# Performance work log

Hardware: AMD Instinct MI355X
Metric: run time of the kernel (lower is better)

Reference implementation:

```python
import jax, jax.numpy as jnp
import numpy as np

NUM_HEADS = 32
NUM_KV_HEADS = 8
HEAD_DIM = 64
D_MODEL = 2048
N_REP = NUM_HEADS // NUM_KV_HEADS


def _rotate_half(t):
    h = t.shape[-1] // 2
    return jnp.concatenate([-t[..., h:], t[..., :h]], axis=-1)


def _apply_rope(t, cos, sin):
    # t: (B, H, L, hd); cos/sin: (L, hd) -> broadcast over B, H
    return t * cos[None, None, :, :] + _rotate_half(t) * sin[None, None, :, :]


def setup_inputs() -> dict:
    key = jax.random.key(0)
    ks = jax.random.split(key, 7)
    B, L = 2, 2048
    x = jax.random.normal(ks[0], (B, L, D_MODEL), dtype=jnp.float32)
    # RoPE tables (build real rotary tables for realism)
    inv_freq = 1.0 / (10000.0 ** (jnp.arange(0, HEAD_DIM, 2, dtype=jnp.float32) / HEAD_DIM))
    t = jnp.arange(L, dtype=jnp.float32)
    freqs = jnp.outer(t, inv_freq)              # (L, hd/2)
    emb = jnp.concatenate([freqs, freqs], -1)   # (L, hd)
    cos = jnp.cos(emb)
    sin = jnp.sin(emb)
    s = 0.02
    Wq = s * jax.random.normal(ks[1], (D_MODEL, D_MODEL), dtype=jnp.float32)
    Wk = s * jax.random.normal(ks[2], (NUM_KV_HEADS * HEAD_DIM, D_MODEL), dtype=jnp.float32)
    Wv = s * jax.random.normal(ks[3], (NUM_KV_HEADS * HEAD_DIM, D_MODEL), dtype=jnp.float32)
    Wo = s * jax.random.normal(ks[4], (D_MODEL, D_MODEL), dtype=jnp.float32)
    return {"x": x, "cos": cos, "sin": sin, "Wq": Wq, "Wk": Wk, "Wv": Wv, "Wo": Wo}


def reference(x, cos, sin, Wq, Wk, Wv, Wo):
    B, L, _ = x.shape
    # Projections (Linear: y = x @ W^T)
    Q = (x @ Wq.T).reshape(B, L, NUM_HEADS, HEAD_DIM).transpose(0, 2, 1, 3)      # (B,H,L,d)
    K = (x @ Wk.T).reshape(B, L, NUM_KV_HEADS, HEAD_DIM).transpose(0, 2, 1, 3)   # (B,Hk,L,d)
    V = (x @ Wv.T).reshape(B, L, NUM_KV_HEADS, HEAD_DIM).transpose(0, 2, 1, 3)
    Q = _apply_rope(Q, cos, sin)
    K = _apply_rope(K, cos, sin)
    # GQA: group Q heads by kv head instead of materializing repeated K/V
    Qg = Q.reshape(B, NUM_KV_HEADS, N_REP, L, HEAD_DIM)
    scale = 1.0 / jnp.sqrt(jnp.array(HEAD_DIM, dtype=x.dtype))
    scores = jnp.einsum('bgrqd,bgkd->bgrqk', Qg, K) * scale                      # (B,Hk,rep,L,L)
    causal = jnp.tril(jnp.ones((L, L), dtype=bool))
    scores = jnp.where(causal[None, None, None], scores, jnp.finfo(scores.dtype).min)
    probs = jax.nn.softmax(scores, axis=-1)
    out = jnp.einsum('bgrqk,bgkd->bgrqd', probs, V)                              # (B,Hk,rep,L,d)
    out = out.reshape(B, NUM_HEADS, L, HEAD_DIM).transpose(0, 2, 1, 3).reshape(B, L, D_MODEL)
    return out @ Wo.T
```

## Files before the change

### kernel.cpp

```cpp
#include <hip/hip_runtime.h>
#include <stdint.h>

#define B_   2
#define L_   2048
#define DM   2048
#define NH   32
#define NKV  8
#define HD   64

typedef __attribute__((ext_vector_type(8))) short short8;
typedef __attribute__((ext_vector_type(4))) float f32x4;
typedef __attribute__((ext_vector_type(16))) float f32x16;

__device__ __forceinline__ unsigned short f2b(float f) {
  union { float f; unsigned int u; } x; x.f = f;
  unsigned int u = x.u + 0x7fffu + ((x.u >> 16) & 1u);
  return (unsigned short)(u >> 16);
}

__device__ __forceinline__ void gload16(const void* g, void* l) {
  __builtin_amdgcn_global_load_lds((const __attribute__((address_space(1))) void*)(g),
                                   (__attribute__((address_space(3))) void*)(l), 16, 0, 0);
}

__device__ __forceinline__ unsigned int cvtpk_bf16(float a, float b) {
  unsigned int r;
  asm("v_cvt_pk_bf16_f32 %0, %1, %2" : "=v"(r) : "v"(a), "v"(b));
  return r;
}

__device__ __forceinline__ void pl32swap(unsigned int& a, unsigned int& b) {
  asm("v_permlane32_swap_b32 %0, %1" : "+v"(a), "+v"(b));
}

#if __has_builtin(__builtin_amdgcn_exp2f)
__device__ __forceinline__ float fexp2(float x) { return __builtin_amdgcn_exp2f(x); }
#else
__device__ __forceinline__ float fexp2(float x) {
  float r; asm("v_exp_f32 %0, %1" : "=v"(r) : "v"(x)); return r;
}
#endif

union U8 { unsigned int u[4]; short8 s; };

__global__ void conv_all(const float* __restrict__ x,  const float* __restrict__ Wq,
                         const float* __restrict__ Wk, const float* __restrict__ Wv,
                         const float* __restrict__ Wo,
                         unsigned short* __restrict__ xb, unsigned short* __restrict__ wqkv,
                         unsigned short* __restrict__ wo) {
  int u = blockIdx.x * blockDim.x + threadIdx.x;
  const float* s;
  unsigned short* d;
  if (u < 2097152)            { s = x  + (size_t)u * 4;               d = xb + (size_t)u * 4; }
  else if (u < 3145728)       { s = Wq + (size_t)(u - 2097152) * 4;   d = wqkv + (size_t)(u - 2097152) * 4; }
  else if (u < 3407872)       { s = Wk + (size_t)(u - 3145728) * 4;   d = wqkv + 4194304 + (size_t)(u - 3145728) * 4; }
  else if (u < 3670016)       { s = Wv + (size_t)(u - 3407872) * 4;   d = wqkv + 5242880 + (size_t)(u - 3407872) * 4; }
  else                        { s = Wo + (size_t)(u - 3670016) * 4;   d = wo + (size_t)(u - 3670016) * 4; }
  float4 v = *(const float4*)s;
  ushort4 o;
  o.x = f2b(v.x); o.y = f2b(v.y); o.z = f2b(v.z); o.w = f2b(v.w);
  *(ushort4*)d = o;
}

#define GSTAGE4(SM, BUF, K0)                                                    \
  {                                                                             \
    unsigned short* Ad = (SM) + (BUF) * 8192;                                   \
    gload16(Ab + (size_t)srow * K + (K0) + scolz,        Ad + w * 512);         \
    gload16(Ab + (size_t)(srow + 64) * K + (K0) + scolz, Ad + 2048 + w * 512);  \
    gload16(Bb + (size_t)srow * K + (K0) + scolz,        Ad + 4096 + w * 512);  \
    gload16(Bb + (size_t)(srow + 64) * K + (K0) + scolz, Ad + 6144 + w * 512);  \
  }

__global__ __launch_bounds__(256) void gemm_bt(const unsigned short* __restrict__ A,
                                               const unsigned short* __restrict__ Bw,
                                               float* __restrict__ C,
                                               int M, int N, int K) {
  __shared__ unsigned short sm[3 * 8192];
  const int tid = threadIdx.x;
  const int w = tid >> 6, l = tid & 63;
  const int lo = l & 15, hi = l >> 4;
  const int xcd = blockIdx.x & 7;
  const int wi = blockIdx.x >> 3;
  const int bm = (xcd >> 1) * 8 + (wi >> 3);
  const int bn = (xcd & 1) * 8 + (wi & 7);
  const int wm = w >> 1, wn = w & 1;
  f32x4 acc[4][4] = {};
  const unsigned short* Ab = A + (size_t)(bm * 128) * K;
  const unsigned short* Bb = Bw + (size_t)(bn * 128) * K;
  const int srow = tid >> 2;
  const int scolz = (((tid & 3) ^ ((tid >> 2) & 3)) * 8);
  const int csw = lo & 3;

  const int nk = K >> 5;
  GSTAGE4(sm, 0, 0);
  GSTAGE4(sm, 1, 32);
  int cur = 0;
  for (int t = 0; t < nk; ++t) {
    if (t + 1 < nk) asm volatile("s_waitcnt vmcnt(4)" ::: "memory");
    else            asm volatile("s_waitcnt vmcnt(0)" ::: "memory");
    __builtin_amdgcn_s_barrier();
    __builtin_amdgcn_sched_barrier(0);
    const int nb2 = (cur + 2 >= 3) ? cur - 1 : cur + 2;
    if (t + 2 < nk) GSTAGE4(sm, nb2, (t + 2) * 32);
    const unsigned short* As = sm + cur * 8192;
    const unsigned short* Bs = As + 4096;
    const int kk = (hi ^ csw) * 8;
    short8 a[4], b[4];
#pragma unroll
    for (int i = 0; i < 4; ++i)
      a[i] = *(const short8*)&As[(wm * 64 + i * 16 + lo) * 32 + kk];
#pragma unroll
    for (int j = 0; j < 4; ++j)
      b[j] = *(const short8*)&Bs[(wn * 64 + j * 16 + lo) * 32 + kk];
    __builtin_amdgcn_s_setprio(1);
#pragma unroll
    for (int i = 0; i < 4; ++i)
#pragma unroll
      for (int j = 0; j < 4; ++j)
        acc[i][j] = __builtin_amdgcn_mfma_f32_16x16x32_bf16(a[i], b[j], acc[i][j], 0, 0, 0);
    __builtin_amdgcn_s_setprio(0);
    cur = (cur + 1 >= 3) ? 0 : cur + 1;
  }
  const int r0 = hi * 4;
#pragma unroll
  for (int i = 0; i < 4; ++i)
#pragma unroll
    for (int j = 0; j < 4; ++j)
#pragma unroll
      for (int r = 0; r < 4; ++r)
        C[(size_t)(bm * 128 + wm * 64 + i * 16 + r0 + r) * N + bn * 128 + wn * 64 + j * 16 + lo] =
            acc[i][j][r];
}

#define GSTAGE8(SM, BUF, K0)                                                    \
  {                                                                             \
    unsigned short* Ad = (SM) + (BUF) * 8192;                                   \
    gload16(Ab + (size_t)srow * K + (K0) + scolz, Ad + w * 512);                \
    gload16(Bb + (size_t)srow * K + (K0) + scolz, Ad + 4096 + w * 512);         \
  }

__global__ __launch_bounds__(512) void gemm_qkv(const unsigned short* __restrict__ A,
                                                const unsigned short* __restrict__ Bw,
                                                const float* __restrict__ cosT,
                                                const float* __restrict__ sinT,
                                                unsigned short* __restrict__ qrope,
                                                unsigned short* __restrict__ krope,
                                                unsigned short* __restrict__ vt) {
  const int K = 2048;
  __shared__ unsigned short sm[3 * 8192];
  const int tid = threadIdx.x;
  const int w = tid >> 6, l = tid & 63;
  const int lo = l & 15, hi = l >> 4;
  const int xcd = blockIdx.x & 7;
  const int wi = blockIdx.x >> 3;
  const int bm = (xcd >> 1) * 8 + wi / 12;
  const int bn = (xcd & 1) * 12 + wi % 12;
  const int wm = w >> 1, wn = w & 1;
  f32x4 acc[2][4] = {};
  const unsigned short* Ab = A + (size_t)(bm * 128) * K;
  const unsigned short* Bb = Bw + (size_t)(bn * 128) * K;
  const int srow = tid >> 2;
  const int scolz = (((tid & 3) ^ ((tid >> 2) & 3)) * 8);
  const int csw = lo & 3;

  const int nk = K >> 5;
  GSTAGE8(sm, 0, 0);
  GSTAGE8(sm, 1, 32);
  int cur = 0;
  for (int t = 0; t < nk; ++t) {
    if (t + 1 < nk) asm volatile("s_waitcnt vmcnt(2)" ::: "memory");
    else            asm volatile("s_waitcnt vmcnt(0)" ::: "memory");
    __builtin_amdgcn_s_barrier();
    __builtin_amdgcn_sched_barrier(0);
    const int nb2 = (cur + 2 >= 3) ? cur - 1 : cur + 2;
    if (t + 2 < nk) GSTAGE8(sm, nb2, (t + 2) * 32);
    const unsigned short* As = sm + cur * 8192;
    const unsigned short* Bs = As + 4096;
    const int kk = (hi ^ csw) * 8;
    short8 a[2], b[4];
#pragma unroll
    for (int i = 0; i < 2; ++i)
      a[i] = *(const short8*)&As[(wm * 32 + i * 16 + lo) * 32 + kk];
#pragma unroll
    for (int j = 0; j < 4; ++j)
      b[j] = *(const short8*)&Bs[(wn * 64 + j * 16 + lo) * 32 + kk];
    __builtin_amdgcn_s_setprio(1);
#pragma unroll
    for (int i = 0; i < 2; ++i)
#pragma unroll
      for (int j = 0; j < 4; ++j)
        acc[i][j] = __builtin_amdgcn_mfma_f32_16x16x32_bf16(a[i], b[j], acc[i][j], 0, 0, 0);
    __builtin_amdgcn_s_setprio(0);
    cur = (cur + 1 >= 3) ? 0 : cur + 1;
  }

  __syncthreads();
  unsigned short* T = sm;
  const float SC = 0.18033688011112042f;
  if (bn < 16) {
#pragma unroll
    for (int i = 0; i < 2; ++i)
#pragma unroll
      for (int r = 0; r < 4; ++r) {
        const int tr = wm * 32 + i * 16 + hi * 4 + r;
        const int lpos = (bm * 128 + tr) & (L_ - 1);
        const float* cr = cosT + lpos * 64;
        const float* sr = sinT + lpos * 64;
        float q0 = acc[i][0][r], q1 = acc[i][1][r], q2 = acc[i][2][r], q3 = acc[i][3][r];
        unsigned short* tp = T + tr * 132 + wn * 64 + lo;
        tp[0]  = f2b((q0 * cr[lo]      - q2 * sr[lo])      * SC);
        tp[16] = f2b((q1 * cr[lo + 16] - q3 * sr[lo + 16]) * SC);
        tp[32] = f2b((q2 * cr[lo + 32] + q0 * sr[lo + 32]) * SC);
        tp[48] = f2b((q3 * cr[lo + 48] + q1 * sr[lo + 48]) * SC);
      }
  } else if (bn < 20) {
#pragma unroll
    for (int i = 0; i < 2; ++i)
#pragma unroll
      for (int r = 0; r < 4; ++r) {
        const int tr = wm * 32 + i * 16 + hi * 4 + r;
        const int lpos = (bm * 128 + tr) & (L_ - 1);
        const float* cr = cosT + lpos * 64;
        const float* sr = sinT + lpos * 64;
        float q0 = acc[i][0][r], q1 = acc[i][1][r], q2 = acc[i][2][r], q3 = acc[i][3][r];
        unsigned short* tp = T + tr * 132 + wn * 64 + lo;
        tp[0]  = f2b(q0 * cr[lo]      - q2 * sr[lo]);
        tp[16] = f2b(q1 * cr[lo + 16] - q3 * sr[lo + 16]);
        tp[32] = f2b(q2 * cr[lo + 32] + q0 * sr[lo + 32]);
        tp[48] = f2b(q3 * cr[lo + 48] + q1 * sr[lo + 48]);
      }
  } else {
#pragma unroll
    for (int i = 0; i < 2; ++i)
#pragma unroll
      for (int r = 0; r < 4; ++r) {
        const int tr = wm * 32 + i * 16 + hi * 4 + r;
        unsigned short* tp = T + tr * 132 + wn * 64 + lo;
#pragma unroll
        for (int j = 0; j < 4; ++j)
          tp[j * 16] = f2b(acc[i][j][r]);
      }
  }
  __syncthreads();

  const int bb = bm >> 4;
  const int lp0 = (bm & 15) * 128;
  if (bn < 20) {
    unsigned short* base = (bn < 16) ? qrope : krope;
    const int nheads = (bn < 16) ? NH : NKV;
    const int h0 = (bn < 16) ? bn * 2 : (bn - 16) * 2;
#pragma unroll
    for (int it = 0; it < 4; ++it) {
      const int tr2 = it * 32 + (tid >> 4);
      const int c = (tid & 15) * 8;
      short8 v = *(const short8*)(T + tr2 * 132 + c);
      const int hl = c >> 6, d8 = c & 63;
      *(short8*)(base + ((size_t)(bb * nheads + h0 + hl) * L_ + lp0 + tr2) * 64 + d8) = v;
    }
  } else {
    const int g0 = (bn - 20) * 2;
#pragma unroll
    for (int it = 0; it < 4; ++it) {
      const int dl = it * 32 + (tid >> 4);
      const int ch = (tid & 15) * 8;
      U8 v;
#pragma unroll
      for (int k2 = 0; k2 < 4; ++k2) {
        unsigned short e0 = T[(ch + 2 * k2) * 132 + dl];
        unsigned short e1 = T[(ch + 2 * k2 + 1) * 132 + dl];
        v.u[k2] = (unsigned int)e0 | ((unsigned int)e1 << 16);
      }
      const int gl = dl >> 6, d = dl & 63;
      *(short8*)(vt + ((size_t)((bb * NKV + g0 + gl) * HD + d)) * L_ + lp0 + ch) = v.s;
    }
  }
}

__global__ __launch_bounds__(256) void attn(const unsigned short* __restrict__ Qb,
                                            const unsigned short* __restrict__ Kb,
                                            const unsigned short* __restrict__ Vtb,
                                            unsigned short* __restrict__ AO) {
  __shared__ unsigned short smem[3 * 8192];
  const int h = blockIdx.y, b = blockIdx.z;
  const int g = h >> 2;
  const int tid = threadIdx.x;
  const int w = tid >> 6, l = tid & 63;
  const int q5 = l & 31, hi2 = l >> 5;

  const unsigned short* Qh = Qb + (size_t)(b * NH + h) * L_ * HD;
  const char* Kg = (const char*)(Kb + (size_t)(b * NKV + g) * L_ * HD);
  const char* Vg = (const char*)(Vtb + (size_t)(b * NKV + g) * HD * L_);

  const int r8 = l >> 3;
  const int swz_src = ((l & 7) ^ r8) * 16;
  const int myswz = (q5 & 7) << 4;

  const int koff0 = (w * 16 + r8) * 128 + swz_src;
  const int koff1 = koff0 + 1024;
  const int voff0 = (w * 16 + r8) * 4096 + swz_src;
  const int voff1 = voff0 + 32768;
  const int dA0 = w * 1024;
  const int dA1 = dA0 + 512;

  int cA[4];
#pragma unroll
  for (int sc = 0; sc < 4; ++sc) cA[sc] = (sc * 32 + hi2 * 16) ^ myswz;
  const int rK = q5 * 128;

  short8 av2c;
#pragma unroll
  for (int j = 0; j < 8; ++j) av2c[j] = (q5 == 0) ? (short)0x3F80 : (short)0;

#define STAGE2(BUF)                                            \
  {                                                            \
    unsigned short* Kd = smem + (BUF) * 8192;                  \
    gload16(kgp + koff0, Kd + dA0);                            \
    gload16(kgp + koff1, Kd + dA1);                            \
    gload16(vgp + voff0, Kd + 4096 + dA0);                     \
    gload16(vgp + voff1, Kd + 4096 + dA1);                     \
  }

  for (int pass = 0; pass < 2; ++pass) {
    const int qb = pass ? 15 - blockIdx.x : blockIdx.x;
    const unsigned short* Qp = Qh + (size_t)(qb * 128) * HD;

    short8 bq[4];
#pragma unroll
    for (int sc = 0; sc < 4; ++sc)
      bq[sc] = *(const short8*)(Qp + (w * 32 + q5) * HD + sc * 16 + hi2 * 8);

    f32x16 o0 = {}, o1 = {}, o2 = {};
    const int qg = qb * 128 + w * 32 + q5;

    const char* kgp = Kg;
    const char* vgp = Vg;

    const int nt = 2 * qb + 2;
    STAGE2(0);
    kgp += 8192; vgp += 128;
    int cur = 0;
    for (int kt = 0; kt < nt; ++kt) {
      const int nb = (cur == 2) ? 0 : cur + 1;
      if (kt + 1 < nt) {
        STAGE2(nb);
        kgp += 8192; vgp += 128;
        asm volatile("s_waitcnt vmcnt(4)" ::: "memory");
      } else {
        asm volatile("s_waitcnt vmcnt(0)" ::: "memory");
      }
      __builtin_amdgcn_s_barrier();
      __builtin_amdgcn_sched_barrier(0);

      const char* kb = (const char*)smem + cur * 16384 + rK;
      const bool active = (kt * 64 <= qb * 128 + w * 32 + 31);
      if (active) {
        f32x16 s0 = {}, s1 = {};
        __builtin_amdgcn_s_setprio(1);
#pragma unroll
        for (int sc = 0; sc < 4; ++sc) {
          short8 ak = *(const short8*)(kb + cA[sc]);
          s0 = __builtin_amdgcn_mfma_f32_32x32x16_bf16(ak, bq[sc], s0, 0, 0, 0);
        }
#pragma unroll
        for (int sc = 0; sc < 4; ++sc) {
          short8 ak = *(const short8*)(kb + 4096 + cA[sc]);
          s1 = __builtin_amdgcn_mfma_f32_32x32x16_bf16(ak, bq[sc], s1, 0, 0, 0);
        }
        __builtin_amdgcn_s_setprio(0);
        if (kt >= 2 * qb) {
#pragma unroll
          for (int r = 0; r < 16; ++r) {
            const int krow = (r & 3) + 8 * (r >> 2) + 4 * hi2;
            if (kt * 64 + krow > qg)      s0[r] = -1e30f;
            if (kt * 64 + 32 + krow > qg) s1[r] = -1e30f;
          }
        }
#pragma unroll
        for (int r = 0; r < 16; ++r) s0[r] = fexp2(s0[r]);
#pragma unroll
        for (int r = 0; r < 16; ++r) s1[r] = fexp2(s1[r]);
        unsigned int pa[4][4];
#define PACK8(S, Bq, OUT)                                        \
        {                                                        \
          unsigned int u0 = cvtpk_bf16(S[Bq + 0], S[Bq + 1]);    \
          unsigned int u1 = cvtpk_bf16(S[Bq + 2], S[Bq + 3]);    \
          unsigned int u2 = cvtpk_bf16(S[Bq + 4], S[Bq + 5]);    \
          unsigned int u3 = cvtpk_bf16(S[Bq + 6], S[Bq + 7]);    \
          pl32swap(u0, u2); pl32swap(u1, u3);                    \
          OUT[0] = u0; OUT[1] = u1; OUT[2] = u2; OUT[3] = u3;    \
        }
        PACK8(s0, 0, pa[0]); PACK8(s0, 8, pa[1]);
        PACK8(s1, 0, pa[2]); PACK8(s1, 8, pa[3]);
#undef PACK8
        __builtin_amdgcn_s_setprio(1);
#pragma unroll
        for (int kc = 0; kc < 4; ++kc) {
          U8 p; p.u[0] = pa[kc][0]; p.u[1] = pa[kc][1]; p.u[2] = pa[kc][2]; p.u[3] = pa[kc][3];
          short8 av0 = *(const short8*)(kb + 8192 + cA[kc]);
          o0 = __builtin_amdgcn_mfma_f32_32x32x16_bf16(av0, p.s, o0, 0, 0, 0);
          short8 av1 = *(const short8*)(kb + 12288 + cA[kc]);
          o1 = __builtin_amdgcn_mfma_f32_32x32x16_bf16(av1, p.s, o1, 0, 0, 0);
          o2 = __builtin_amdgcn_mfma_f32_32x32x16_bf16(av2c, p.s, o2, 0, 0, 0);
        }
        __builtin_amdgcn_s_setprio(0);
      }
      cur = nb;
    }

    __builtin_amdgcn_s_barrier();

    const float ls = o2[0] + __shfl_xor(o2[0], 32);
    const float inv = 1.f / ls;
    o0 *= inv;
    o1 *= inv;
    const int qrow = w * 32 + q5;
#pragma unroll
    for (int df = 0; df < 2; ++df) {
      const f32x16& o = df ? o1 : o0;
#pragma unroll
      for (int gq = 0; gq < 4; ++gq) {
        unsigned int ulo = cvtpk_bf16(o[4 * gq + 0], o[4 * gq + 1]);
        unsigned int uhi = cvtpk_bf16(o[4 * gq + 2], o[4 * gq + 3]);
        const int colb = df * 64 + gq * 16 + hi2 * 8;
        *(unsigned long long*)((char*)smem + qrow * 128 + (colb ^ myswz)) =
            ((unsigned long long)uhi << 32) | (unsigned long long)ulo;
      }
    }
    __syncthreads();
#pragma unroll
    for (int it = 0; it < 4; ++it) {
      const int row = it * 32 + (tid >> 3);
      const int colb = (tid & 7) * 16;
      short8 v = *(const short8*)((const char*)smem + row * 128 + (colb ^ ((row & 7) << 4)));
      *(short8*)((char*)AO + ((size_t)(b * L_ + qb * 128 + row) * 2048 + h * 64) * 2 + colb) = v;
    }
    __syncthreads();
  }
#undef STAGE2
}

extern "C" void kernel_launch(void* const* d_in, const int* in_sizes, int n_in,
                              void* d_out, int out_size, void* d_ws, size_t ws_size,
                              hipStream_t stream) {
  const float* x    = (const float*)d_in[0];
  const float* cosT = (const float*)d_in[1];
  const float* sinT = (const float*)d_in[2];
  const float* Wq   = (const float*)d_in[3];
  const float* Wk   = (const float*)d_in[4];
  const float* Wv   = (const float*)d_in[5];
  const float* Wo   = (const float*)d_in[6];
  float* out = (float*)d_out;

  char* ws = (char*)d_ws;
  unsigned short* xb    = (unsigned short*)ws;
  unsigned short* wqkv  = xb + 8388608;
  unsigned short* wo    = wqkv + 6291456;
  unsigned short* qrope = wo + 4194304;
  unsigned short* krope = qrope + 8388608;
  unsigned short* vt    = krope + 2097152;
  unsigned short* ao    = vt + 2097152;

  conv_all<<<18432, 256, 0, stream>>>(x, Wq, Wk, Wv, Wo, xb, wqkv, wo);

  gemm_qkv<<<768, 512, 0, stream>>>(xb, wqkv, cosT, sinT, qrope, krope, vt);

  attn<<<dim3(8, 32, 2), 256, 0, stream>>>(qrope, krope, vt, ao);

  gemm_bt<<<512, 256, 0, stream>>>(ao, wo, out, 4096, 2048, 2048);
}
```

Baseline: 182.5 us.

## Fuse x fp32-to-bf16 conversion into QKV GEMM operand load

Removes the separate conversion of activations x to bf16 in the prep kernel. The QKV GEMM now streams fp32 x tiles into LDS with a new XOR swizzle and converts them to bf16 with packed cvt when loading MFMA A fragments. This drops a 16MB read and 8MB write/read round trip of xb. In exchange, each QKV block fetches twice the A bytes from global memory, LDS use grows by half, and conversion instructions are added to the inner loop.

```diff
diff --git a/kernel.cpp b/kernel.cpp
--- a/kernel.cpp
+++ b/kernel.cpp
@@ -43,19 +43,16 @@
 
 union U8 { unsigned int u[4]; short8 s; };
 
-__global__ void conv_all(const float* __restrict__ x,  const float* __restrict__ Wq,
-                         const float* __restrict__ Wk, const float* __restrict__ Wv,
-                         const float* __restrict__ Wo,
-                         unsigned short* __restrict__ xb, unsigned short* __restrict__ wqkv,
-                         unsigned short* __restrict__ wo) {
+__global__ void conv_all(const float* __restrict__ Wq, const float* __restrict__ Wk,
+                         const float* __restrict__ Wv, const float* __restrict__ Wo,
+                         unsigned short* __restrict__ wqkv, unsigned short* __restrict__ wo) {
   int u = blockIdx.x * blockDim.x + threadIdx.x;
   const float* s;
   unsigned short* d;
-  if (u < 2097152)            { s = x  + (size_t)u * 4;               d = xb + (size_t)u * 4; }
-  else if (u < 3145728)       { s = Wq + (size_t)(u - 2097152) * 4;   d = wqkv + (size_t)(u - 2097152) * 4; }
-  else if (u < 3407872)       { s = Wk + (size_t)(u - 3145728) * 4;   d = wqkv + 4194304 + (size_t)(u - 3145728) * 4; }
-  else if (u < 3670016)       { s = Wv + (size_t)(u - 3407872) * 4;   d = wqkv + 5242880 + (size_t)(u - 3407872) * 4; }
-  else                        { s = Wo + (size_t)(u - 3670016) * 4;   d = wo + (size_t)(u - 3670016) * 4; }
+  if (u < 1048576)       { s = Wq + (size_t)u * 4;             d = wqkv + (size_t)u * 4; }
+  else if (u < 1310720)  { s = Wk + (size_t)(u - 1048576) * 4; d = wqkv + 4194304 + (size_t)(u - 1048576) * 4; }
+  else if (u < 1572864)  { s = Wv + (size_t)(u - 1310720) * 4; d = wqkv + 5242880 + (size_t)(u - 1310720) * 4; }
+  else                   { s = Wo + (size_t)(u - 1572864) * 4; d = wo + (size_t)(u - 1572864) * 4; }
   float4 v = *(const float4*)s;
   ushort4 o;
   o.x = f2b(v.x); o.y = f2b(v.y); o.z = f2b(v.z); o.w = f2b(v.w);
@@ -132,14 +129,15 @@
             acc[i][j][r];
 }
 
-#define GSTAGE8(SM, BUF, K0)                                                    \
-  {                                                                             \
-    unsigned short* Ad = (SM) + (BUF) * 8192;                                   \
-    gload16(Ab + (size_t)srow * K + (K0) + scolz, Ad + w * 512);                \
-    gload16(Bb + (size_t)srow * K + (K0) + scolz, Ad + 4096 + w * 512);         \
-  }
-
-__global__ __launch_bounds__(512) void gemm_qkv(const unsigned short* __restrict__ A,
+#define GSTAGEQ(SM, BUF, K0)                                                       \
+  {                                                                                \
+    unsigned short* Ad = (SM) + (BUF) * 12288;                                     \
+    gload16(Af + (size_t)(aRow)*2048 + (K0) + acol,        Ad + w * 512);          \
+    gload16(Af + (size_t)(aRow + 64)*2048 + (K0) + acol,   Ad + 4096 + w * 512);   \
+    gload16(Bb + (size_t)srow * 2048 + (K0) + scolz,       Ad + 8192 + w * 512);   \
+  }
+
+__global__ __launch_bounds__(512) void gemm_qkv(const float* __restrict__ X,
                                                 const unsigned short* __restrict__ Bw,
                                                 const float* __restrict__ cosT,
                                                 const float* __restrict__ sinT,
@@ -147,7 +145,7 @@
                                                 unsigned short* __restrict__ krope,
                                                 unsigned short* __restrict__ vt) {
   const int K = 2048;
-  __shared__ unsigned short sm[3 * 8192];
+  __shared__ unsigned short sm[3 * 12288];
   const int tid = threadIdx.x;
   const int w = tid >> 6, l = tid & 63;
   const int lo = l & 15, hi = l >> 4;
@@ -157,30 +155,42 @@
   const int bn = (xcd & 1) * 12 + wi % 12;
   const int wm = w >> 1, wn = w & 1;
   f32x4 acc[2][4] = {};
-  const unsigned short* Ab = A + (size_t)(bm * 128) * K;
+  const float* Af = X + (size_t)(bm * 128) * K;
   const unsigned short* Bb = Bw + (size_t)(bn * 128) * K;
+  const int aRow = w * 8 + (l >> 3);
+  const int acol = ((l & 7) ^ ((l >> 3) & 7)) * 4;
   const int srow = tid >> 2;
   const int scolz = (((tid & 3) ^ ((tid >> 2) & 3)) * 8);
   const int csw = lo & 3;
+  const int aswr = lo & 7;
 
   const int nk = K >> 5;
-  GSTAGE8(sm, 0, 0);
-  GSTAGE8(sm, 1, 32);
+  GSTAGEQ(sm, 0, 0);
+  GSTAGEQ(sm, 1, 32);
   int cur = 0;
   for (int t = 0; t < nk; ++t) {
-    if (t + 1 < nk) asm volatile("s_waitcnt vmcnt(2)" ::: "memory");
+    if (t + 1 < nk) asm volatile("s_waitcnt vmcnt(3)" ::: "memory");
     else            asm volatile("s_waitcnt vmcnt(0)" ::: "memory");
     __builtin_amdgcn_s_barrier();
     __builtin_amdgcn_sched_barrier(0);
     const int nb2 = (cur + 2 >= 3) ? cur - 1 : cur + 2;
-    if (t + 2 < nk) GSTAGE8(sm, nb2, (t + 2) * 32);
-    const unsigned short* As = sm + cur * 8192;
-    const unsigned short* Bs = As + 4096;
+    if (t + 2 < nk) GSTAGEQ(sm, nb2, (t + 2) * 32);
+    const float* Asf = (const float*)(sm + cur * 12288);
+    const unsigned short* Bs = sm + cur * 12288 + 8192;
+    short8 a[2], b[4];
+#pragma unroll
+    for (int i = 0; i < 2; ++i) {
+      const int rowA = wm * 32 + i * 16 + lo;
+      f32x4 f0 = *(const f32x4*)(Asf + rowA * 32 + (((2 * hi) ^ aswr) << 2));
+      f32x4 f1 = *(const f32x4*)(Asf + rowA * 32 + (((2 * hi + 1) ^ aswr) << 2));
+      U8 ua;
+      ua.u[0] = cvtpk_bf16(f0[0], f0[1]);
+      ua.u[1] = cvtpk_bf16(f0[2], f0[3]);
+      ua.u[2] = cvtpk_bf16(f1[0], f1[1]);
+      ua.u[3] = cvtpk_bf16(f1[2], f1[3]);
+      a[i] = ua.s;
+    }
     const int kk = (hi ^ csw) * 8;
-    short8 a[2], b[4];
-#pragma unroll
-    for (int i = 0; i < 2; ++i)
-      a[i] = *(const short8*)&As[(wm * 32 + i * 16 + lo) * 32 + kk];
 #pragma unroll
     for (int j = 0; j < 4; ++j)
       b[j] = *(const short8*)&Bs[(wn * 64 + j * 16 + lo) * 32 + kk];
@@ -452,17 +462,16 @@
   float* out = (float*)d_out;
 
   char* ws = (char*)d_ws;
-  unsigned short* xb    = (unsigned short*)ws;
-  unsigned short* wqkv  = xb + 8388608;
+  unsigned short* wqkv  = (unsigned short*)ws;
   unsigned short* wo    = wqkv + 6291456;
   unsigned short* qrope = wo + 4194304;
   unsigned short* krope = qrope + 8388608;
   unsigned short* vt    = krope + 2097152;
   unsigned short* ao    = vt + 2097152;
 
-  conv_all<<<18432, 256, 0, stream>>>(x, Wq, Wk, Wv, Wo, xb, wqkv, wo);
-
-  gemm_qkv<<<768, 512, 0, stream>>>(xb, wqkv, cosT, sinT, qrope, krope, vt);
+  conv_all<<<10240, 256, 0, stream>>>(Wq, Wk, Wv, Wo, wqkv, wo);
+
+  gemm_qkv<<<768, 512, 0, stream>>>(x, wqkv, cosT, sinT, qrope, krope, vt);
 
   attn<<<dim3(8, 32, 2), 256, 0, stream>>>(qrope, krope, vt, ao);
 
```

Result: slower. 189.0 us (+3.6%).
